# Kernel tuning notes

Measured on AMD Instinct MI355X. Metric: run time of the kernel, lower is better.

The kernel has to match this reference:

```python
import jax, jax.numpy as jnp
import numpy as np

B, T, EMB, H = 4, 2048, 1024, 16
S = EMB // H


def setup_inputs() -> dict:
    key = jax.random.key(0)
    ks = jax.random.split(key, 7)
    x = jax.random.normal(ks[0], (B, T, EMB), dtype=jnp.float32)
    pad_amounts = jax.random.randint(ks[1], (B,), 0, 512, dtype=jnp.int64)
    Wk = jax.random.normal(ks[2], (S, S), dtype=jnp.float32) * (1.0 / np.sqrt(S))
    Wq = jax.random.normal(ks[3], (S, S), dtype=jnp.float32) * (1.0 / np.sqrt(S))
    Wv = jax.random.normal(ks[4], (S, S), dtype=jnp.float32) * (1.0 / np.sqrt(S))
    Wu = jax.random.normal(ks[5], (EMB, EMB), dtype=jnp.float32) * (1.0 / np.sqrt(EMB))
    bu = jax.random.normal(ks[6], (EMB,), dtype=jnp.float32) * 0.01
    return {"x": x, "Wk": Wk, "Wq": Wq, "Wv": Wv, "Wu": Wu, "bu": bu,
            "pad_amounts": pad_amounts}


def reference(x, Wk, Wq, Wv, Wu, bu, pad_amounts):
    b, t, e = x.shape
    h = H
    s = e // h
    xh = x.reshape(b, t, h, s)
    # torch Linear: y = x @ W.T (no bias for k/q/v)
    keys = jnp.einsum('bths,os->btho', xh, Wk)
    queries = jnp.einsum('bths,os->btho', xh, Wq)
    values = jnp.einsum('bths,os->btho', xh, Wv)
    # (b,t,h,s) -> (b*h,t,s)
    keys = keys.transpose(0, 2, 1, 3).reshape(b * h, t, s)
    queries = queries.transpose(0, 2, 1, 3).reshape(b * h, t, s)
    values = values.transpose(0, 2, 1, 3).reshape(b * h, t, s)
    scale = e ** 0.25
    queries = queries / scale
    keys = keys / scale
    dot = jnp.einsum('nqs,nks->nqk', queries, keys)  # (b*h, t, t)
    # Faithful to original bug: only the first b flat indices of b*h get masked.
    pad_full = jnp.concatenate([pad_amounts,
                                jnp.zeros(b * h - b, dtype=pad_amounts.dtype)])
    thresh = (t - pad_full)[:, None, None]  # (b*h,1,1); thresh=t -> no mask
    pos = jnp.arange(t)
    mask = (pos[None, :, None] >= thresh) & (pos[None, None, :] >= thresh)
    dot = jnp.where(mask, -jnp.inf, dot)
    att = jax.nn.softmax(dot, axis=2)
    out = jnp.einsum('nqk,nks->nqs', att, values)  # (b*h,t,s)
    out = out.reshape(b, h, t, s).transpose(0, 2, 1, 3).reshape(b, t, h * s)
    return out @ Wu.T + bu
```

## Files before the change

### kernel.cpp

```cpp
#include <hip/hip_runtime.h>


typedef float f32x4 __attribute__((ext_vector_type(4)));
typedef float f32x16 __attribute__((ext_vector_type(16)));
typedef _Float16 f16x2 __attribute__((ext_vector_type(2)));
typedef _Float16 f16x8 __attribute__((ext_vector_type(8)));
typedef unsigned u32x4 __attribute__((ext_vector_type(4)));

#define MFMA16(a, b, c) __builtin_amdgcn_mfma_f32_16x16x32_f16((a), (b), (c), 0, 0, 0)
#define MFMA32(a, b, c) __builtin_amdgcn_mfma_f32_32x32x16_f16((a), (b), (c), 0, 0, 0)

constexpr int Tn = 2048;
constexpr int Bn = 4;
constexpr int EMBn = 1024;
constexpr float NEG_INF = -3.0e38f;

__device__ __forceinline__ float exp2_hw(float x) {
  float r; asm("v_exp_f32 %0, %1" : "=v"(r) : "v"(x)); return r;
}
__device__ __forceinline__ unsigned pkrtz(float lo, float hi) {
  unsigned r; asm("v_cvt_pkrtz_f16_f32 %0, %1, %2" : "=v"(r) : "v"(lo), "v"(hi)); return r;
}
__device__ __forceinline__ unsigned pkadd(unsigned a, unsigned b) {
  unsigned r; asm("v_pk_add_f16 %0, %1, %2" : "=v"(r) : "v"(a), "v"(b)); return r;
}
__device__ __forceinline__ void permswap(unsigned& a, unsigned& b) {
  asm("v_permlane32_swap_b32 %0, %1" : "+v"(a), "+v"(b));
}
__device__ __forceinline__ void glds16(const void* g, void* l) {
  __builtin_amdgcn_global_load_lds(
      (const __attribute__((address_space(1))) unsigned*)g,
      (__attribute__((address_space(3))) unsigned*)l, 16, 0, 0);
}

__global__ __launch_bounds__(256) void sa_prep(
    const float* __restrict__ Wk, const float* __restrict__ Wq,
    const float* __restrict__ Wv, const float* __restrict__ Wu,
    _Float16* __restrict__ w3, _Float16* __restrict__ wub) {
  int idx = blockIdx.x * 256 + threadIdx.x;
  const float rs = 0.21233046f;
  if (idx < 1048576) wub[idx] = (_Float16)Wu[idx];
  if (idx < 4096) {
    w3[idx]        = (_Float16)(Wk[idx] * rs);
    w3[4096 + idx] = (_Float16)(Wq[idx] * rs);
    w3[8192 + idx] = (_Float16)(Wv[idx]);
  }
}

__global__ __launch_bounds__(256) void sa_qkv(
    const float* __restrict__ x, const _Float16* __restrict__ w3,
    _Float16* __restrict__ Qb, _Float16* __restrict__ Kb, _Float16* __restrict__ Vt) {
  const int wave = threadIdx.x >> 6;
  const int lane = threadIdx.x & 63;
  const int g = lane >> 4, c = lane & 15;
  const int n = blockIdx.y, b = n >> 4, h = n & 15;
  const int t0 = blockIdx.x * 64 + wave * 16;

  f16x8 ax[2];
#pragma unroll
  for (int kk = 0; kk < 2; ++kk) {
    const float* xp = x + ((long)((b * Tn + t0 + c) * 16 + h)) * 64 + kk * 32 + g * 8;
    f32x4 u = *(const f32x4*)xp;
    f32x4 v = *(const f32x4*)(xp + 4);
    f16x8 a;
    a[0] = (_Float16)u[0]; a[1] = (_Float16)u[1]; a[2] = (_Float16)u[2]; a[3] = (_Float16)u[3];
    a[4] = (_Float16)v[0]; a[5] = (_Float16)v[1]; a[6] = (_Float16)v[2]; a[7] = (_Float16)v[3];
    ax[kk] = a;
  }

#pragma unroll
  for (int w = 0; w < 2; ++w) {
    _Float16* dst = w ? Qb : Kb;
#pragma unroll
    for (int ot = 0; ot < 4; ++ot) {
      f32x4 a_ = {0.f, 0.f, 0.f, 0.f};
#pragma unroll
      for (int kk = 0; kk < 2; ++kk) {
        f16x8 wf = *(const f16x8*)(w3 + w * 4096 + (ot * 16 + c) * 64 + kk * 32 + g * 8);
        a_ = MFMA16(ax[kk], wf, a_);
      }
#pragma unroll
      for (int r = 0; r < 4; ++r)
        dst[((long)n * Tn + t0 + g * 4 + r) * 64 + ot * 16 + c] = (_Float16)a_[r];
    }
  }

#pragma unroll
  for (int ot = 0; ot < 4; ++ot) {
    f32x4 a_ = {0.f, 0.f, 0.f, 0.f};
#pragma unroll
    for (int kk = 0; kk < 2; ++kk) {
      f16x8 wf = *(const f16x8*)(w3 + 8192 + (ot * 16 + c) * 64 + kk * 32 + g * 8);
      a_ = MFMA16(wf, ax[kk], a_);
    }
#pragma unroll
    for (int r = 0; r < 4; ++r)
      Vt[((long)n * 64 + ot * 16 + g * 4 + r) * Tn + t0 + c] = (_Float16)a_[r];
  }
}

__global__ __launch_bounds__(256, 2) void sa_flash(
    const _Float16* __restrict__ Qb, const _Float16* __restrict__ Kb,
    const _Float16* __restrict__ Vt, const int* __restrict__ pad32,
    _Float16* __restrict__ AO) {
  const int bid = blockIdx.x;
  const int n = (bid & 7) * 8 + (bid >> 6);
  const int qblk = (bid >> 3) & 7;
  const int tid = threadIdx.x;
  const int wave = tid >> 6;
  const int lane = tid & 63;
  const int ql = lane & 31;
  const int hi = lane >> 5;

  int thresh = Tn;
  if (n < Bn) {
    bool is64 = (pad32[1] == 0 && pad32[3] == 0);
    int pv = is64 ? pad32[2 * n] : pad32[n];
    thresh = Tn - pv;
  }

  const int qbase = qblk * 256 + wave * 64;
  const _Float16* Qh = Qb + (long)n * Tn * 64;
  const _Float16* Kh = Kb + (long)n * Tn * 64;
  const _Float16* Vh = Vt + (long)n * 64 * Tn;

  f16x8 bq[2][4];
#pragma unroll
  for (int qh = 0; qh < 2; ++qh) {
    const _Float16* qp = Qh + (long)(qbase + qh * 32 + ql) * 64 + hi * 8;
#pragma unroll
    for (int ks = 0; ks < 4; ++ks) bq[qh][ks] = *(const f16x8*)(qp + ks * 16);
  }

  __shared__ __align__(16) char smem[32768];

  const int srow = wave * 16 + (lane >> 3);
  const int sswz = ((lane & 7) ^ (lane >> 3)) * 8;
  const _Float16* ksrc = Kh + (long)srow * 64 + sswz;
  const _Float16* vsrc = Vh + (long)srow * Tn + sswz;

  f32x16 o[2][2];
  f32x16 zf;
#pragma unroll
  for (int i = 0; i < 16; ++i) {
    o[0][0][i] = 0.f; o[0][1][i] = 0.f; o[1][0][i] = 0.f; o[1][1][i] = 0.f;
    zf[i] = 0.f;
  }
  float l0 = 0.f, l1 = 0.f;

  const bool qge0 = (qbase + ql) >= thresh;
  const bool qge1 = (qbase + 32 + ql) >= thresh;
  const bool qany = (qbase + 64) > thresh;
  const int sw = ql & 7;

  {
    char* kd = smem + wave * 2048;
    char* vd = smem + 16384 + wave * 2048;
    glds16(ksrc, kd);
    glds16(ksrc + 512, kd + 1024);
    glds16(vsrc, vd);
    glds16(vsrc + 8 * Tn, vd + 1024);
  }
  __syncthreads();

  int cur = 0;
  for (int kb = 0; kb < Tn; kb += 64) {
    const int kbn = (kb + 64) & (Tn - 1);
    {
      char* kd = smem + (cur ^ 1) * 8192 + wave * 2048;
      char* vd = smem + 16384 + (cur ^ 1) * 8192 + wave * 2048;
      glds16(ksrc + kbn * 64, kd);
      glds16(ksrc + kbn * 64 + 512, kd + 1024);
      glds16(vsrc + kbn, vd);
      glds16(vsrc + kbn + 8 * Tn, vd + 1024);
    }

    const char* kbb = smem + cur * 8192;
    const char* vbb = smem + 16384 + cur * 8192;

#pragma unroll
    for (int sub = 0; sub < 2; ++sub) {
      const char* krow = kbb + (sub * 32 + ql) * 128;
      f16x8 ka0 = *(const f16x8*)(krow + (((0 + hi) ^ sw) * 16));
      f16x8 ka1 = *(const f16x8*)(krow + (((2 + hi) ^ sw) * 16));
      f16x8 ka2 = *(const f16x8*)(krow + (((4 + hi) ^ sw) * 16));
      f16x8 ka3 = *(const f16x8*)(krow + (((6 + hi) ^ sw) * 16));

      __builtin_amdgcn_s_setprio(1);
      f32x16 st0 = MFMA32(ka0, bq[0][0], zf);
      f32x16 st1 = MFMA32(ka0, bq[1][0], zf);
      st0 = MFMA32(ka1, bq[0][1], st0);
      st1 = MFMA32(ka1, bq[1][1], st1);
      st0 = MFMA32(ka2, bq[0][2], st0);
      st1 = MFMA32(ka2, bq[1][2], st1);
      st0 = MFMA32(ka3, bq[0][3], st0);
      st1 = MFMA32(ka3, bq[1][3], st1);
      __builtin_amdgcn_s_setprio(0);

      if (qany && (kb + sub * 32 + 32) > thresh) {
#pragma unroll
        for (int r = 0; r < 16; ++r) {
          int kr_ = kb + sub * 32 + (r & 3) + 8 * (r >> 2) + 4 * hi;
          if (kr_ >= thresh) {
            if (qge0) st0[r] = NEG_INF;
            if (qge1) st1[r] = NEG_INF;
          }
        }
      }

      const char* vrow0 = vbb + ql * 128;
      const char* vrow1 = vbb + (ql + 32) * 128;
      f16x8 va0 = *(const f16x8*)(vrow0 + (((sub * 4 + hi) ^ sw) * 16));
      f16x8 va1 = *(const f16x8*)(vrow0 + (((sub * 4 + 2 + hi) ^ sw) * 16));
      f16x8 va2 = *(const f16x8*)(vrow1 + (((sub * 4 + hi) ^ sw) * 16));
      f16x8 va3 = *(const f16x8*)(vrow1 + (((sub * 4 + 2 + hi) ^ sw) * 16));

#pragma unroll
      for (int qh = 0; qh < 2; ++qh) {
        const f32x16& stq = qh ? st1 : st0;
        float p[16];
#pragma unroll
        for (int r = 0; r < 16; ++r) p[r] = exp2_hw(stq[r]);

        unsigned pw[8], psum[2];
#pragma unroll
        for (int j = 0; j < 2; ++j) {
          unsigned a0 = pkrtz(p[j * 8 + 0], p[j * 8 + 1]);
          unsigned b0 = pkrtz(p[j * 8 + 4], p[j * 8 + 5]);
          unsigned a1 = pkrtz(p[j * 8 + 2], p[j * 8 + 3]);
          unsigned b1 = pkrtz(p[j * 8 + 6], p[j * 8 + 7]);
          psum[j] = pkadd(pkadd(a0, b0), pkadd(a1, b1));
          permswap(a0, b0);
          permswap(a1, b1);
          pw[j * 4 + 0] = a0; pw[j * 4 + 1] = a1;
          pw[j * 4 + 2] = b0; pw[j * 4 + 3] = b1;
        }
        {
          f16x2 ph = __builtin_bit_cast(f16x2, pkadd(psum[0], psum[1]));
          if (qh) l1 += (float)ph[0] + (float)ph[1];
          else    l0 += (float)ph[0] + (float)ph[1];
        }
        u32x4 u0 = {pw[0], pw[1], pw[2], pw[3]};
        u32x4 u1 = {pw[4], pw[5], pw[6], pw[7]};
        f16x8 pb0 = __builtin_bit_cast(f16x8, u0);
        f16x8 pb1 = __builtin_bit_cast(f16x8, u1);

        __builtin_amdgcn_s_setprio(1);
        o[qh][0] = MFMA32(va0, pb0, o[qh][0]);
        o[qh][0] = MFMA32(va1, pb1, o[qh][0]);
        o[qh][1] = MFMA32(va2, pb0, o[qh][1]);
        o[qh][1] = MFMA32(va3, pb1, o[qh][1]);
        __builtin_amdgcn_s_setprio(0);
      }
    }

    __syncthreads();
    cur ^= 1;
  }

  float lf0 = l0 + __shfl_xor(l0, 32, 64);
  float lf1 = l1 + __shfl_xor(l1, 32, 64);
  float linv0 = 1.0f / lf0;
  float linv1 = 1.0f / lf1;

  const int bb = n >> 4, hh = n & 15;
  const int qr = lane >> 3, s0 = (lane & 7) * 8;
  _Float16* my = (_Float16*)(smem + wave * 8192);
#pragma unroll
  for (int qh = 0; qh < 2; ++qh) {
    float linv = qh ? linv1 : linv0;
    _Float16* myq = my + qh * 2048;
#pragma unroll
    for (int stile = 0; stile < 2; ++stile) {
#pragma unroll
      for (int r = 0; r < 16; r += 2) {
        unsigned wv = pkrtz(o[qh][stile][r] * linv, o[qh][stile][r + 1] * linv);
        int s = stile * 32 + (r & 3) + 8 * (r >> 2) + 4 * hi;
        *(unsigned*)(myq + ql * 64 + (s ^ ((ql & 7) << 3))) = wv;
      }
    }
  }
  asm volatile("s_waitcnt lgkmcnt(0)" ::: "memory");

#pragma unroll
  for (int qh = 0; qh < 2; ++qh) {
    _Float16* myq = my + qh * 2048;
#pragma unroll
    for (int j = 0; j < 4; ++j) {
      int q = j * 8 + qr;
      f16x8 vv = *(const f16x8*)(myq + q * 64 + (s0 ^ ((q & 7) << 3)));
      *(f16x8*)(AO + ((long)(bb * Tn + qbase + qh * 32 + q)) * EMBn + hh * 64 + s0) = vv;
    }
  }
}

__global__ __launch_bounds__(256, 4) void sa_oproj(
    const _Float16* __restrict__ A, const _Float16* __restrict__ WuB,
    const float* __restrict__ bu, float* __restrict__ Y) {
  const int bid = blockIdx.x;
  const int xcd = bid & 7;
  const int j = bid >> 3;
  const int nstrip = j & 15;
  const int mblk = xcd * 8 + (j >> 4);
  const int tid = threadIdx.x;
  const int wave = tid >> 6;
  const int lane = tid & 63;
  const int ql = lane & 31;
  const int hi = lane >> 5;
  const int mbase = mblk * 128 + wave * 32;
  const int nbase = nstrip * 64;

  __shared__ __align__(16) char bsm[18432];
  const int sr = tid >> 3, sc = tid & 7;
  const _Float16* wg0 = WuB + (long)(nbase + sr) * 1024 + sc * 8;
  const _Float16* wg1 = WuB + (long)(nbase + sr + 32) * 1024 + sc * 8;
  char* ww0 = bsm + sr * 144 + sc * 16;
  char* ww1 = bsm + (sr + 32) * 144 + sc * 16;

  const _Float16* ap = A + (long)(mbase + ql) * 1024 + hi * 8;

  f32x16 acc[2];
#pragma unroll
  for (int i = 0; i < 16; ++i) { acc[0][i] = 0.f; acc[1][i] = 0.f; }

  {
    f16x8 w0 = *(const f16x8*)wg0;
    f16x8 w1 = *(const f16x8*)wg1;
    *(f16x8*)ww0 = w0;
    *(f16x8*)ww1 = w1;
  }
  __syncthreads();

  int cur = 0;
  for (int kb = 0; kb < 1024; kb += 64) {
    const int kbn = (kb + 64) & 1023;
    f16x8 wn0 = *(const f16x8*)(wg0 + kbn);
    f16x8 wn1 = *(const f16x8*)(wg1 + kbn);

    f16x8 af[4];
#pragma unroll
    for (int ks = 0; ks < 4; ++ks) af[ks] = *(const f16x8*)(ap + kb + ks * 16);

    const char* bbase = bsm + cur * 9216;
#pragma unroll
    for (int nt = 0; nt < 2; ++nt) {
      const char* brow = bbase + (nt * 32 + ql) * 144;
#pragma unroll
      for (int ks = 0; ks < 4; ++ks) {
        f16x8 bf = *(const f16x8*)(brow + (ks * 2 + hi) * 16);
        acc[nt] = MFMA32(af[ks], bf, acc[nt]);
      }
    }

    *(f16x8*)(ww0 + (cur ^ 1) * 9216) = wn0;
    *(f16x8*)(ww1 + (cur ^ 1) * 9216) = wn1;
    __syncthreads();
    cur ^= 1;
  }

#pragma unroll
  for (int nt = 0; nt < 2; ++nt) {
    float bias = bu[nbase + nt * 32 + ql];
#pragma unroll
    for (int r = 0; r < 16; ++r) {
      int mrow = mbase + (r & 3) + 8 * (r >> 2) + 4 * hi;
      Y[(long)mrow * 1024 + nbase + nt * 32 + ql] = acc[nt][r] + bias;
    }
  }
}

extern "C" void kernel_launch(void* const* d_in, const int* in_sizes, int n_in,
                              void* d_out, int out_size, void* d_ws, size_t ws_size,
                              hipStream_t stream) {
  const float* x  = (const float*)d_in[0];
  const float* Wk = (const float*)d_in[1];
  const float* Wq = (const float*)d_in[2];
  const float* Wv = (const float*)d_in[3];
  const float* Wu = (const float*)d_in[4];
  const float* bu = (const float*)d_in[5];
  const int* pad  = (const int*)d_in[6];
  float* Y = (float*)d_out;

  _Float16* ws  = (_Float16*)d_ws;
  _Float16* w3  = ws;
  _Float16* wub = ws + 16384;
  _Float16* Qb  = ws + 16384 + 1048576;
  _Float16* Kb  = Qb + 8388608;
  _Float16* Vt  = Kb + 8388608;
  _Float16* AO  = Vt + 8388608;

  sa_prep<<<4096, 256, 0, stream>>>(Wk, Wq, Wv, Wu, w3, wub);
  sa_qkv<<<dim3(32, 64), 256, 0, stream>>>(x, w3, Qb, Kb, Vt);
  sa_flash<<<dim3(512), 256, 0, stream>>>(Qb, Kb, Vt, pad, AO);
  sa_oproj<<<dim3(1024), 256, 0, stream>>>(AO, wub, bu, Y);
}
```

Baseline: 148.6 us.

## Stage QKV outputs through LDS for coalesced stores; double M tile in oproj

The QKV projection kernel now writes K, Q and transposed V tiles into padded shared memory, then stores them to global memory as coalesced 16-byte vectors. Before, each lane wrote scattered 2-byte values, which was especially costly for the transposed V. The output projection now has each wave compute a 64x64 tile instead of 32x64, so every B fragment read from LDS feeds twice as many MFMAs. Its grid is halved and occupancy lowered to 2 blocks per CU, trading more accumulator registers and less parallelism for better reuse.

```diff
diff --git a/kernel.cpp b/kernel.cpp
--- a/kernel.cpp
+++ b/kernel.cpp
@@ -50,16 +50,23 @@
 __global__ __launch_bounds__(256) void sa_qkv(
     const float* __restrict__ x, const _Float16* __restrict__ w3,
     _Float16* __restrict__ Qb, _Float16* __restrict__ Kb, _Float16* __restrict__ Vt) {
-  const int wave = threadIdx.x >> 6;
-  const int lane = threadIdx.x & 63;
+  const int tid = threadIdx.x;
+  const int wave = tid >> 6;
+  const int lane = tid & 63;
   const int g = lane >> 4, c = lane & 15;
   const int n = blockIdx.y, b = n >> 4, h = n & 15;
-  const int t0 = blockIdx.x * 64 + wave * 16;
+  const int t0 = blockIdx.x * 64;
+  const int tw = t0 + wave * 16;
+
+  __shared__ __align__(16) _Float16 sm[3 * 64 * 72];
+  _Float16* smK = sm;
+  _Float16* smQ = sm + 4608;
+  _Float16* smV = sm + 9216;
 
   f16x8 ax[2];
 #pragma unroll
   for (int kk = 0; kk < 2; ++kk) {
-    const float* xp = x + ((long)((b * Tn + t0 + c) * 16 + h)) * 64 + kk * 32 + g * 8;
+    const float* xp = x + ((long)((b * Tn + tw + c) * 16 + h)) * 64 + kk * 32 + g * 8;
     f32x4 u = *(const f32x4*)xp;
     f32x4 v = *(const f32x4*)(xp + 4);
     f16x8 a;
@@ -70,7 +77,7 @@
 
 #pragma unroll
   for (int w = 0; w < 2; ++w) {
-    _Float16* dst = w ? Qb : Kb;
+    _Float16* dst = w ? smQ : smK;
 #pragma unroll
     for (int ot = 0; ot < 4; ++ot) {
       f32x4 a_ = {0.f, 0.f, 0.f, 0.f};
@@ -81,7 +88,7 @@
       }
 #pragma unroll
       for (int r = 0; r < 4; ++r)
-        dst[((long)n * Tn + t0 + g * 4 + r) * 64 + ot * 16 + c] = (_Float16)a_[r];
+        dst[(wave * 16 + g * 4 + r) * 72 + ot * 16 + c] = (_Float16)a_[r];
     }
   }
 
@@ -95,7 +102,21 @@
     }
 #pragma unroll
     for (int r = 0; r < 4; ++r)
-      Vt[((long)n * 64 + ot * 16 + g * 4 + r) * Tn + t0 + c] = (_Float16)a_[r];
+      smV[(ot * 16 + g * 4 + r) * 72 + wave * 16 + c] = (_Float16)a_[r];
+  }
+
+  __syncthreads();
+
+  const int sl = tid & 7;
+#pragma unroll
+  for (int j = 0; j < 2; ++j) {
+    int row = j * 32 + (tid >> 3);
+    f16x8 kv = *(const f16x8*)(smK + row * 72 + sl * 8);
+    f16x8 qv = *(const f16x8*)(smQ + row * 72 + sl * 8);
+    f16x8 vv = *(const f16x8*)(smV + row * 72 + sl * 8);
+    *(f16x8*)(Kb + ((long)n * Tn + t0 + row) * 64 + sl * 8) = kv;
+    *(f16x8*)(Qb + ((long)n * Tn + t0 + row) * 64 + sl * 8) = qv;
+    *(f16x8*)(Vt + ((long)n * 64 + row) * Tn + t0 + sl * 8) = vv;
   }
 }
 
@@ -294,20 +315,20 @@
   }
 }
 
-__global__ __launch_bounds__(256, 4) void sa_oproj(
+__global__ __launch_bounds__(256, 2) void sa_oproj(
     const _Float16* __restrict__ A, const _Float16* __restrict__ WuB,
     const float* __restrict__ bu, float* __restrict__ Y) {
   const int bid = blockIdx.x;
   const int xcd = bid & 7;
   const int j = bid >> 3;
   const int nstrip = j & 15;
-  const int mblk = xcd * 8 + (j >> 4);
+  const int mblk = xcd * 4 + (j >> 4);
   const int tid = threadIdx.x;
   const int wave = tid >> 6;
   const int lane = tid & 63;
   const int ql = lane & 31;
   const int hi = lane >> 5;
-  const int mbase = mblk * 128 + wave * 32;
+  const int mbase = mblk * 256 + wave * 64;
   const int nbase = nstrip * 64;
 
   __shared__ __align__(16) char bsm[18432];
@@ -317,11 +338,14 @@
   char* ww0 = bsm + sr * 144 + sc * 16;
   char* ww1 = bsm + (sr + 32) * 144 + sc * 16;
 
-  const _Float16* ap = A + (long)(mbase + ql) * 1024 + hi * 8;
-
-  f32x16 acc[2];
-#pragma unroll
-  for (int i = 0; i < 16; ++i) { acc[0][i] = 0.f; acc[1][i] = 0.f; }
+  const _Float16* ap0 = A + (long)(mbase + ql) * 1024 + hi * 8;
+  const _Float16* ap1 = ap0 + 32 * 1024;
+
+  f32x16 acc[2][2];
+#pragma unroll
+  for (int i = 0; i < 16; ++i) {
+    acc[0][0][i] = 0.f; acc[0][1][i] = 0.f; acc[1][0][i] = 0.f; acc[1][1][i] = 0.f;
+  }
 
   {
     f16x8 w0 = *(const f16x8*)wg0;
@@ -337,19 +361,22 @@
     f16x8 wn0 = *(const f16x8*)(wg0 + kbn);
     f16x8 wn1 = *(const f16x8*)(wg1 + kbn);
 
-    f16x8 af[4];
-#pragma unroll
-    for (int ks = 0; ks < 4; ++ks) af[ks] = *(const f16x8*)(ap + kb + ks * 16);
+    f16x8 af0[4], af1[4];
+#pragma unroll
+    for (int ks = 0; ks < 4; ++ks) {
+      af0[ks] = *(const f16x8*)(ap0 + kb + ks * 16);
+      af1[ks] = *(const f16x8*)(ap1 + kb + ks * 16);
+    }
 
     const char* bbase = bsm + cur * 9216;
 #pragma unroll
-    for (int nt = 0; nt < 2; ++nt) {
-      const char* brow = bbase + (nt * 32 + ql) * 144;
-#pragma unroll
-      for (int ks = 0; ks < 4; ++ks) {
-        f16x8 bf = *(const f16x8*)(brow + (ks * 2 + hi) * 16);
-        acc[nt] = MFMA32(af[ks], bf, acc[nt]);
-      }
+    for (int ks = 0; ks < 4; ++ks) {
+      f16x8 b0 = *(const f16x8*)(bbase + ql * 144 + (ks * 2 + hi) * 16);
+      f16x8 b1 = *(const f16x8*)(bbase + (32 + ql) * 144 + (ks * 2 + hi) * 16);
+      acc[0][0] = MFMA32(af0[ks], b0, acc[0][0]);
+      acc[0][1] = MFMA32(af0[ks], b1, acc[0][1]);
+      acc[1][0] = MFMA32(af1[ks], b0, acc[1][0]);
+      acc[1][1] = MFMA32(af1[ks], b1, acc[1][1]);
     }
 
     *(f16x8*)(ww0 + (cur ^ 1) * 9216) = wn0;
@@ -359,12 +386,15 @@
   }
 
 #pragma unroll
-  for (int nt = 0; nt < 2; ++nt) {
-    float bias = bu[nbase + nt * 32 + ql];
-#pragma unroll
-    for (int r = 0; r < 16; ++r) {
-      int mrow = mbase + (r & 3) + 8 * (r >> 2) + 4 * hi;
-      Y[(long)mrow * 1024 + nbase + nt * 32 + ql] = acc[nt][r] + bias;
+  for (int nf = 0; nf < 2; ++nf) {
+    float bias = bu[nbase + nf * 32 + ql];
+#pragma unroll
+    for (int mf = 0; mf < 2; ++mf) {
+#pragma unroll
+      for (int r = 0; r < 16; ++r) {
+        int mrow = mbase + mf * 32 + (r & 3) + 8 * (r >> 2) + 4 * hi;
+        Y[(long)mrow * 1024 + nbase + nf * 32 + ql] = acc[mf][nf][r] + bias;
+      }
     }
   }
 }
@@ -392,5 +422,5 @@
   sa_prep<<<4096, 256, 0, stream>>>(Wk, Wq, Wv, Wu, w3, wub);
   sa_qkv<<<dim3(32, 64), 256, 0, stream>>>(x, w3, Qb, Kb, Vt);
   sa_flash<<<dim3(512), 256, 0, stream>>>(Qb, Kb, Vt, pad, AO);
-  sa_oproj<<<dim3(1024), 256, 0, stream>>>(AO, wub, bu, Y);
-}
+  sa_oproj<<<dim3(512), 256, 0, stream>>>(AO, wub, bu, Y);
+}
```

Measured after the change: 158.6 us. +6.8%, slower.
